# Kernel tuning notes

Hardware: AMD Instinct MI355X
Metric: run time of the kernel (lower is better)

Reference implementation:

```python
import jax, jax.numpy as jnp
import numpy as np

B = 8192      # contrastive batch size
D = 64        # embedding dim
TEMP = 0.07   # temperature (init kwarg)
EPS = 1e-8    # F.cosine_similarity eps
N_CLASSES = 1000


def setup_inputs() -> dict:
    key = jax.random.key(0)
    k1, k2, k3 = jax.random.split(key, 3)
    return {
        "label_tensor": jax.random.randint(k1, (B,), 0, N_CLASSES),
        "feature_a": jax.random.normal(k2, (B, D), dtype=jnp.float32),
        "feature_b": jax.random.normal(k3, (B, D), dtype=jnp.float32),
    }


def reference(label_tensor, feature_a, feature_b):
    # cos_score[i, j] = cosine(feature_a[i], feature_b[j])  -> [B, B]
    na = jnp.maximum(jnp.linalg.norm(feature_a, axis=1), EPS)  # [B]
    nb = jnp.maximum(jnp.linalg.norm(feature_b, axis=1), EPS)  # [B]
    cos_score = (feature_a @ feature_b.T) / (na[:, None] * nb[None, :])

    # cross_modality=True (feature_b given): no diagonal exclusion.
    e = jnp.exp(cos_score / TEMP)                               # [B, B]
    same = label_tensor[:, None] == label_tensor[None, :]       # [B, B] bool
    numerator = jnp.sum(jnp.where(same, e, 0.0), axis=1)        # [B]
    denominator = jnp.sum(e, axis=1)                            # [B]
    # original: if numerator == 0: numerator += 0.01
    numerator = jnp.where(numerator == 0.0, numerator + 0.01, numerator)
    loss = -jnp.mean(jnp.log(numerator / denominator))
    return (loss.reshape(1), cos_score)
```

## Files before the change

kernel.cpp:

```cpp
#include <hip/hip_runtime.h>
#include <hip/hip_bf16.h>

#define BATCH 8192
#define DIM 64
#define INV_TEMP 14.2857142857142857f
#define EPS_NORM 1e-8f

typedef __attribute__((ext_vector_type(8))) short bf16x8;
typedef __attribute__((ext_vector_type(4))) float f32x4;

__device__ __forceinline__ unsigned short f2bf_rne(float x) {
  unsigned int u = __float_as_uint(x);
  u += 0x7FFFu + ((u >> 16) & 1u);
  return (unsigned short)(u >> 16);
}

__global__ __launch_bounds__(256) void norm_kernel(
    const float* __restrict__ A, const float* __restrict__ Bm,
    unsigned short* __restrict__ An, unsigned short* __restrict__ Bn,
    float* __restrict__ numer, float* __restrict__ denom) {
  int gid  = blockIdx.x * 256 + threadIdx.x;
  int row  = gid >> 6;
  int lane = gid & 63;
  float a = A[row * DIM + lane];
  float b = Bm[row * DIM + lane];
  float sa = a * a, sb = b * b;
#pragma unroll
  for (int m = 32; m; m >>= 1) {
    sa += __shfl_xor(sa, m);
    sb += __shfl_xor(sb, m);
  }
  float ia = 1.0f / fmaxf(sqrtf(sa), EPS_NORM);
  float ib = 1.0f / fmaxf(sqrtf(sb), EPS_NORM);
  An[row * DIM + lane] = f2bf_rne(a * ia);
  Bn[row * DIM + lane] = f2bf_rne(b * ib);
  if (lane == 0) {
    numer[row] = 0.0f;
    denom[row] = 0.0f;
  }
}

__global__ __launch_bounds__(256) void cos_mfma_kernel(
    const unsigned short* __restrict__ An, const unsigned short* __restrict__ Bn,
    const int* __restrict__ labels,
    float* __restrict__ numer, float* __restrict__ denom,
    float* __restrict__ cos_out) {
  const int tid  = threadIdx.x;
  const int lane = tid & 63;
  const int wave = tid >> 6;
  const int wr = wave >> 1, wc = wave & 1;
  const int m = lane & 15, q = lane >> 4;
  const int row0 = blockIdx.y * 128 + wr * 64;
  const int col0 = blockIdx.x * 128 + wc * 64;

  bf16x8 afr[4][2], bfr[4][2];
#pragma unroll
  for (int t = 0; t < 4; ++t) {
    const unsigned short* ap = An + (size_t)(row0 + t * 16 + m) * DIM + q * 8;
    const unsigned short* bp = Bn + (size_t)(col0 + t * 16 + m) * DIM + q * 8;
#pragma unroll
    for (int h = 0; h < 2; ++h) {
      afr[t][h] = *(const bf16x8*)(ap + h * 32);
      bfr[t][h] = *(const bf16x8*)(bp + h * 32);
    }
  }

  f32x4 acc[4][4];
#pragma unroll
  for (int mt = 0; mt < 4; ++mt)
#pragma unroll
    for (int nt = 0; nt < 4; ++nt) {
      f32x4 a = {0.f, 0.f, 0.f, 0.f};
      a = __builtin_amdgcn_mfma_f32_16x16x32_bf16(afr[mt][0], bfr[nt][0], a, 0, 0, 0);
      a = __builtin_amdgcn_mfma_f32_16x16x32_bf16(afr[mt][1], bfr[nt][1], a, 0, 0, 0);
      acc[mt][nt] = a;
    }

  int labc[4];
#pragma unroll
  for (int nt = 0; nt < 4; ++nt) labc[nt] = labels[col0 + nt * 16 + m];
  int lrw[4][4];
#pragma unroll
  for (int mt = 0; mt < 4; ++mt) {
    int lr = labels[row0 + mt * 16 + m];
#pragma unroll
    for (int i = 0; i < 4; ++i) lrw[mt][i] = __shfl(lr, q * 4 + i);
  }

  float es[4][4], ns[4][4];
#pragma unroll
  for (int mt = 0; mt < 4; ++mt)
#pragma unroll
    for (int i = 0; i < 4; ++i) { es[mt][i] = 0.f; ns[mt][i] = 0.f; }

#pragma unroll
  for (int mt = 0; mt < 4; ++mt) {
#pragma unroll
    for (int nt = 0; nt < 4; ++nt) {
#pragma unroll
      for (int i = 0; i < 4; ++i) {
        float c = acc[mt][nt][i];
        size_t row = (size_t)(row0 + mt * 16 + q * 4 + i);
        __builtin_nontemporal_store(c, cos_out + row * BATCH + col0 + nt * 16 + m);
        float e = __expf(c * INV_TEMP);
        es[mt][i] += e;
        if (labc[nt] == lrw[mt][i]) ns[mt][i] += e;
      }
    }
  }

#pragma unroll
  for (int mt = 0; mt < 4; ++mt)
#pragma unroll
    for (int i = 0; i < 4; ++i) {
      float e = es[mt][i], n = ns[mt][i];
#pragma unroll
      for (int msk = 1; msk < 16; msk <<= 1) {
        e += __shfl_xor(e, msk);
        n += __shfl_xor(n, msk);
      }
      es[mt][i] = e; ns[mt][i] = n;
    }

  __shared__ float redN[2][128], redD[2][128];
  if (m == 0) {
#pragma unroll
    for (int mt = 0; mt < 4; ++mt)
#pragma unroll
      for (int i = 0; i < 4; ++i) {
        int r = wr * 64 + mt * 16 + q * 4 + i;
        redN[wc][r] = ns[mt][i];
        redD[wc][r] = es[mt][i];
      }
  }
  __syncthreads();
  if (tid < 128) {
    int row = blockIdx.y * 128 + tid;
    atomicAdd(&numer[row], redN[0][tid] + redN[1][tid]);
    atomicAdd(&denom[row], redD[0][tid] + redD[1][tid]);
  }
}

__global__ __launch_bounds__(256) void loss_kernel(
    const float* __restrict__ numer, const float* __restrict__ denom,
    float* __restrict__ out) {
  __shared__ float red[4];
  float s = 0.0f;
  for (int i = threadIdx.x; i < BATCH; i += 256) {
    float n = numer[i];
    n = (n == 0.0f) ? (n + 0.01f) : n;
    s += logf(n / denom[i]);
  }
#pragma unroll
  for (int m = 32; m; m >>= 1) s += __shfl_xor(s, m);
  if ((threadIdx.x & 63) == 0) red[threadIdx.x >> 6] = s;
  __syncthreads();
  if (threadIdx.x == 0) {
    float t = red[0] + red[1] + red[2] + red[3];
    out[0] = -t / (float)BATCH;
  }
}

extern "C" void kernel_launch(void* const* d_in, const int* in_sizes, int n_in,
                              void* d_out, int out_size, void* d_ws, size_t ws_size,
                              hipStream_t stream) {
  const int*   labels = (const int*)d_in[0];
  const float* A      = (const float*)d_in[1];
  const float* Bf     = (const float*)d_in[2];
  float* out = (float*)d_out;

  unsigned short* An = (unsigned short*)d_ws;
  unsigned short* Bn = An + BATCH * DIM;
  float* numer = (float*)(Bn + BATCH * DIM);
  float* denom = numer + BATCH;

  hipLaunchKernelGGL(norm_kernel, dim3(BATCH * 64 / 256), dim3(256), 0, stream,
                     A, Bf, An, Bn, numer, denom);
  hipLaunchKernelGGL(cos_mfma_kernel, dim3(BATCH / 128, BATCH / 128), dim3(256),
                     0, stream, An, Bn, labels, numer, denom, out + 1);
  hipLaunchKernelGGL(loss_kernel, dim3(1), dim3(256), 0, stream,
                     numer, denom, out);
}
```

Baseline: 414.7 us.

## Loop over column tiles per block and replace atomics with partial-sum buffers

```diff
diff --git a/kernel.cpp b/kernel.cpp
--- a/kernel.cpp
+++ b/kernel.cpp
@@ -1,10 +1,11 @@
 #include <hip/hip_runtime.h>
-#include <hip/hip_bf16.h>
 
 #define BATCH 8192
 #define DIM 64
 #define INV_TEMP 14.2857142857142857f
 #define EPS_NORM 1e-8f
+#define NXB 8
+#define CT_PER_BLOCK 8
 
 typedef __attribute__((ext_vector_type(8))) short bf16x8;
 typedef __attribute__((ext_vector_type(4))) float f32x4;
@@ -18,7 +19,7 @@
 __global__ __launch_bounds__(256) void norm_kernel(
     const float* __restrict__ A, const float* __restrict__ Bm,
     unsigned short* __restrict__ An, unsigned short* __restrict__ Bn,
-    float* __restrict__ numer, float* __restrict__ denom) {
+    float* __restrict__ out) {
   int gid  = blockIdx.x * 256 + threadIdx.x;
   int row  = gid >> 6;
   int lane = gid & 63;
@@ -34,16 +35,13 @@
   float ib = 1.0f / fmaxf(sqrtf(sb), EPS_NORM);
   An[row * DIM + lane] = f2bf_rne(a * ia);
   Bn[row * DIM + lane] = f2bf_rne(b * ib);
-  if (lane == 0) {
-    numer[row] = 0.0f;
-    denom[row] = 0.0f;
-  }
+  if (gid == 0) out[0] = 0.0f;
 }
 
 __global__ __launch_bounds__(256) void cos_mfma_kernel(
     const unsigned short* __restrict__ An, const unsigned short* __restrict__ Bn,
     const int* __restrict__ labels,
-    float* __restrict__ numer, float* __restrict__ denom,
+    float* __restrict__ pN, float* __restrict__ pD,
     float* __restrict__ cos_out) {
   const int tid  = threadIdx.x;
   const int lane = tid & 63;
@@ -51,34 +49,15 @@
   const int wr = wave >> 1, wc = wave & 1;
   const int m = lane & 15, q = lane >> 4;
   const int row0 = blockIdx.y * 128 + wr * 64;
-  const int col0 = blockIdx.x * 128 + wc * 64;
 
-  bf16x8 afr[4][2], bfr[4][2];
+  bf16x8 afr[4][2];
 #pragma unroll
   for (int t = 0; t < 4; ++t) {
     const unsigned short* ap = An + (size_t)(row0 + t * 16 + m) * DIM + q * 8;
-    const unsigned short* bp = Bn + (size_t)(col0 + t * 16 + m) * DIM + q * 8;
 #pragma unroll
-    for (int h = 0; h < 2; ++h) {
-      afr[t][h] = *(const bf16x8*)(ap + h * 32);
-      bfr[t][h] = *(const bf16x8*)(bp + h * 32);
-    }
+    for (int h = 0; h < 2; ++h) afr[t][h] = *(const bf16x8*)(ap + h * 32);
   }
 
-  f32x4 acc[4][4];
-#pragma unroll
-  for (int mt = 0; mt < 4; ++mt)
-#pragma unroll
-    for (int nt = 0; nt < 4; ++nt) {
-      f32x4 a = {0.f, 0.f, 0.f, 0.f};
-      a = __builtin_amdgcn_mfma_f32_16x16x32_bf16(afr[mt][0], bfr[nt][0], a, 0, 0, 0);
-      a = __builtin_amdgcn_mfma_f32_16x16x32_bf16(afr[mt][1], bfr[nt][1], a, 0, 0, 0);
-      acc[mt][nt] = a;
-    }
-
-  int labc[4];
-#pragma unroll
-  for (int nt = 0; nt < 4; ++nt) labc[nt] = labels[col0 + nt * 16 + m];
   int lrw[4][4];
 #pragma unroll
   for (int mt = 0; mt < 4; ++mt) {
@@ -93,18 +72,36 @@
 #pragma unroll
     for (int i = 0; i < 4; ++i) { es[mt][i] = 0.f; ns[mt][i] = 0.f; }
 
+  for (int ct = 0; ct < CT_PER_BLOCK; ++ct) {
+    const int col0 = (blockIdx.x * CT_PER_BLOCK + ct) * 128 + wc * 64;
+
+    bf16x8 bfr[4][2];
 #pragma unroll
-  for (int mt = 0; mt < 4; ++mt) {
+    for (int t = 0; t < 4; ++t) {
+      const unsigned short* bp = Bn + (size_t)(col0 + t * 16 + m) * DIM + q * 8;
 #pragma unroll
-    for (int nt = 0; nt < 4; ++nt) {
+      for (int h = 0; h < 2; ++h) bfr[t][h] = *(const bf16x8*)(bp + h * 32);
+    }
+    int labc[4];
 #pragma unroll
-      for (int i = 0; i < 4; ++i) {
-        float c = acc[mt][nt][i];
-        size_t row = (size_t)(row0 + mt * 16 + q * 4 + i);
-        __builtin_nontemporal_store(c, cos_out + row * BATCH + col0 + nt * 16 + m);
-        float e = __expf(c * INV_TEMP);
-        es[mt][i] += e;
-        if (labc[nt] == lrw[mt][i]) ns[mt][i] += e;
+    for (int nt = 0; nt < 4; ++nt) labc[nt] = labels[col0 + nt * 16 + m];
+
+#pragma unroll
+    for (int mt = 0; mt < 4; ++mt) {
+#pragma unroll
+      for (int nt = 0; nt < 4; ++nt) {
+        f32x4 a = {0.f, 0.f, 0.f, 0.f};
+        a = __builtin_amdgcn_mfma_f32_16x16x32_bf16(afr[mt][0], bfr[nt][0], a, 0, 0, 0);
+        a = __builtin_amdgcn_mfma_f32_16x16x32_bf16(afr[mt][1], bfr[nt][1], a, 0, 0, 0);
+#pragma unroll
+        for (int i = 0; i < 4; ++i) {
+          float c = a[i];
+          size_t row = (size_t)(row0 + mt * 16 + q * 4 + i);
+          cos_out[row * BATCH + col0 + nt * 16 + m] = c;
+          float e = __expf(c * INV_TEMP);
+          es[mt][i] += e;
+          if (labc[nt] == lrw[mt][i]) ns[mt][i] += e;
+        }
       }
     }
   }
@@ -136,28 +133,31 @@
   __syncthreads();
   if (tid < 128) {
     int row = blockIdx.y * 128 + tid;
-    atomicAdd(&numer[row], redN[0][tid] + redN[1][tid]);
-    atomicAdd(&denom[row], redD[0][tid] + redD[1][tid]);
+    pN[(size_t)blockIdx.x * BATCH + row] = redN[0][tid] + redN[1][tid];
+    pD[(size_t)blockIdx.x * BATCH + row] = redD[0][tid] + redD[1][tid];
   }
 }
 
 __global__ __launch_bounds__(256) void loss_kernel(
-    const float* __restrict__ numer, const float* __restrict__ denom,
+    const float* __restrict__ pN, const float* __restrict__ pD,
     float* __restrict__ out) {
-  __shared__ float red[4];
-  float s = 0.0f;
-  for (int i = threadIdx.x; i < BATCH; i += 256) {
-    float n = numer[i];
-    n = (n == 0.0f) ? (n + 0.01f) : n;
-    s += logf(n / denom[i]);
+  int r = blockIdx.x * 256 + threadIdx.x;
+  float n = 0.f, d = 0.f;
+#pragma unroll
+  for (int j = 0; j < NXB; ++j) {
+    n += pN[(size_t)j * BATCH + r];
+    d += pD[(size_t)j * BATCH + r];
   }
+  n = (n == 0.0f) ? (n + 0.01f) : n;
+  float s = logf(n / d);
 #pragma unroll
   for (int m = 32; m; m >>= 1) s += __shfl_xor(s, m);
+  __shared__ float red[4];
   if ((threadIdx.x & 63) == 0) red[threadIdx.x >> 6] = s;
   __syncthreads();
   if (threadIdx.x == 0) {
     float t = red[0] + red[1] + red[2] + red[3];
-    out[0] = -t / (float)BATCH;
+    atomicAdd(out, -t / (float)BATCH);
   }
 }
 
@@ -171,13 +171,13 @@
 
   unsigned short* An = (unsigned short*)d_ws;
   unsigned short* Bn = An + BATCH * DIM;
-  float* numer = (float*)(Bn + BATCH * DIM);
-  float* denom = numer + BATCH;
+  float* pN = (float*)(Bn + BATCH * DIM);
+  float* pD = pN + (size_t)NXB * BATCH;
 
   hipLaunchKernelGGL(norm_kernel, dim3(BATCH * 64 / 256), dim3(256), 0, stream,
-                     A, Bf, An, Bn, numer, denom);
-  hipLaunchKernelGGL(cos_mfma_kernel, dim3(BATCH / 128, BATCH / 128), dim3(256),
-                     0, stream, An, Bn, labels, numer, denom, out + 1);
-  hipLaunchKernelGGL(loss_kernel, dim3(1), dim3(256), 0, stream,
-                     numer, denom, out);
+                     A, Bf, An, Bn, out);
+  hipLaunchKernelGGL(cos_mfma_kernel, dim3(NXB, BATCH / 128), dim3(256),
+                     0, stream, An, Bn, labels, pN, pD, out + 1);
+  hipLaunchKernelGGL(loss_kernel, dim3(BATCH / 256), dim3(256), 0, stream,
+                     pN, pD, out);
 }
```

After: 388.6 us. 6.3% less time.
